# Performance work log

Measured on AMD Instinct MI355X. Metric: run time of the kernel, lower is better.

The kernel has to match this reference:

```python
import jax, jax.numpy as jnp
import numpy as np

NUM_HEADS = 16
HEAD_DIM = 64
WINDOW = 128        # local attention radius |i-j| <= WINDOW
GLOBAL_STRIDE = 64  # tokens at multiples of GLOBAL_STRIDE attend/are attended globally
NEG_INF = -1e9


def sparse_mask(seq_len):
    # bool [S, S]: local band plus global rows/cols (Longformer-style pattern)
    i = jnp.arange(seq_len)
    local = jnp.abs(i[:, None] - i[None, :]) <= WINDOW
    is_global = (i % GLOBAL_STRIDE) == 0
    return local | is_global[:, None] | is_global[None, :]


def setup_inputs() -> dict:
    key = jax.random.key(0)
    k1, k2, k3 = jax.random.split(key, 3)
    B, S, H = 1, 2048, 1024
    x = jax.random.normal(k1, (B, S, H), dtype=jnp.float32)
    Wqkv = jax.random.normal(k2, (3 * H, H), dtype=jnp.float32) * (1.0 / np.sqrt(H))
    Wout = jax.random.normal(k3, (H, H), dtype=jnp.float32) * (1.0 / np.sqrt(H))
    return {"x": x, "Wqkv": Wqkv, "Wout": Wout}


def reference(x, Wqkv, Wout):
    B, S, H = x.shape
    hd = HEAD_DIM
    scale = 1.0 / np.sqrt(hd)

    qkv = x @ Wqkv.T                       # [B, S, 3H] (torch Linear: x @ W^T)
    q, k, v = jnp.split(qkv, 3, axis=-1)
    # [B, nH, S, hd]
    q = q.reshape(B, S, NUM_HEADS, hd).transpose(0, 2, 1, 3)
    k = k.reshape(B, S, NUM_HEADS, hd).transpose(0, 2, 1, 3)
    v = v.reshape(B, S, NUM_HEADS, hd).transpose(0, 2, 1, 3)

    mask = sparse_mask(S)                  # [S, S] bool, broadcasts over (B, nH)
    scores = jnp.einsum('bhqd,bhkd->bhqk', q, k) * scale
    scores = jnp.where(mask, scores, NEG_INF)
    attn = jax.nn.softmax(scores, axis=-1)  # every row has valid keys -> no NaN
    out = jnp.einsum('bhqk,bhkd->bhqd', attn, v)
    out = out.transpose(0, 2, 1, 3).reshape(B, S, H)
    return out @ Wout.T
```

## Files before the change

kernel.cpp:

```cpp
#include <hip/hip_runtime.h>
#include <hip/hip_bf16.h>
#include <math.h>

#define SEQ   2048
#define HID   1024
#define NH    16
#define HD    64
#define WIN   128
#define GSTR  64

typedef __attribute__((ext_vector_type(8))) short short8;
typedef __attribute__((ext_vector_type(4))) float f32x4;
typedef unsigned short ushort_t;

__device__ inline unsigned short bf16b(float f) {
    union { float f; unsigned int u; } v; v.f = f;
    return (unsigned short)((v.u + 0x7FFFu + ((v.u >> 16) & 1u)) >> 16);
}
__device__ inline float blo(unsigned int u) {
    union { unsigned int i; float f; } v; v.i = u << 16; return v.f;
}
__device__ inline float bhi(unsigned int u) {
    union { unsigned int i; float f; } v; v.i = u & 0xFFFF0000u; return v.f;
}

#define GLOAD_LDS16(gp, lp)                                                    \
    __builtin_amdgcn_global_load_lds(                                          \
        (const __attribute__((address_space(1))) unsigned int*)(gp),           \
        (__attribute__((address_space(3))) unsigned int*)(lp), 16, 0, 0)

__global__ __launch_bounds__(256) void cvt_bf16(const float4* __restrict__ x,
                                                const float4* __restrict__ wq,
                                                const float4* __restrict__ wo,
                                                ushort4* __restrict__ x16,
                                                ushort4* __restrict__ wq16,
                                                ushort4* __restrict__ wo16) {
    for (int idx = blockIdx.x * 256 + threadIdx.x; idx < 1572864;
         idx += gridDim.x * 256) {
        const float4* src; ushort4* dst; int off;
        if (idx < 524288)       { src = x;  dst = x16;  off = idx; }
        else if (idx < 1310720) { src = wq; dst = wq16; off = idx - 524288; }
        else                    { src = wo; dst = wo16; off = idx - 1310720; }
        float4 v = src[off];
        ushort4 o;
        o.x = bf16b(v.x); o.y = bf16b(v.y); o.z = bf16b(v.z); o.w = bf16b(v.w);
        dst[off] = o;
    }
}

template <int BM, int BN, typename OT>
__global__ __launch_bounds__(256) void gemm_bt16(const unsigned short* __restrict__ A,
                                                 const unsigned short* __restrict__ B,
                                                 OT* __restrict__ C,
                                                 int M, int N, int K) {
    constexpr int MI = BM / 32;
    constexpr int NJ = BN / 32;
    __shared__ unsigned short As[2][BM * 32];
    __shared__ unsigned short Bs[2][BN * 32];

    const int tid  = threadIdx.x;
    const int wave = tid >> 6;
    const int lane = tid & 63;
    const int quad = lane >> 4;
    const int l15  = lane & 15;
    const int bm = blockIdx.y * BM;
    const int bn = blockIdx.x * BN;
    const int wm = (wave & 1) * (BM / 2);
    const int wn = (wave >> 1) * (BN / 2);
    const int srow = lane >> 2;
    const int scol = (lane & 3) * 8;

    f32x4 acc[MI][NJ];
    #pragma unroll
    for (int i = 0; i < MI; ++i)
        #pragma unroll
        for (int j = 0; j < NJ; ++j)
            acc[i][j] = (f32x4){0.f, 0.f, 0.f, 0.f};

    for (int k0 = 0; k0 < K; k0 += 64) {
        #pragma unroll
        for (int hh = 0; hh < 2; ++hh) {
            #pragma unroll
            for (int t = 0; t < BM / 64; ++t) {
                const int row = wave * (BM / 4) + t * 16 + srow;
                GLOAD_LDS16(A + (size_t)(bm + row) * K + k0 + hh * 32 + scol,
                            &As[hh][(size_t)row * 32 + scol]);
            }
            #pragma unroll
            for (int t = 0; t < BN / 64; ++t) {
                const int row = wave * (BN / 4) + t * 16 + srow;
                GLOAD_LDS16(B + (size_t)(bn + row) * K + k0 + hh * 32 + scol,
                            &Bs[hh][(size_t)row * 32 + scol]);
            }
        }
        __syncthreads();

        #pragma unroll
        for (int hh = 0; hh < 2; ++hh) {
            short8 a[MI], b[NJ];
            #pragma unroll
            for (int im = 0; im < MI; ++im)
                a[im] = *(const short8*)&As[hh][(wm + im * 16 + l15) * 32 + quad * 8];
            #pragma unroll
            for (int jn = 0; jn < NJ; ++jn)
                b[jn] = *(const short8*)&Bs[hh][(wn + jn * 16 + l15) * 32 + quad * 8];

            #pragma unroll
            for (int im = 0; im < MI; ++im)
                #pragma unroll
                for (int jn = 0; jn < NJ; ++jn)
                    acc[im][jn] = __builtin_amdgcn_mfma_f32_16x16x32_bf16(
                        b[jn], a[im], acc[im][jn], 0, 0, 0);
        }
        __syncthreads();
    }

    #pragma unroll
    for (int im = 0; im < MI; ++im)
        #pragma unroll
        for (int jn = 0; jn < NJ; ++jn) {
            const int r = bm + wm + im * 16 + l15;
            const int c = bn + wn + jn * 16 + quad * 4;
            if constexpr (sizeof(OT) == 2) {
                ushort4 o;
                o.x = bf16b(acc[im][jn][0]);
                o.y = bf16b(acc[im][jn][1]);
                o.z = bf16b(acc[im][jn][2]);
                o.w = bf16b(acc[im][jn][3]);
                *(ushort4*)&C[(size_t)r * N + c] = o;
            } else {
                *(f32x4*)&C[(size_t)r * N + c] = acc[im][jn];
            }
        }
}

__global__ __launch_bounds__(256) void attn_fused(const unsigned short* __restrict__ qkv16,
                                                  unsigned short* __restrict__ aout16) {
    __shared__ __align__(16) unsigned char smem[38912];
    const int tid = threadIdx.x;
    const int h = blockIdx.y;
    const int w    = tid >> 6;
    const int lane = tid & 63;
    const int quad = lane >> 4;
    const int l15  = lane & 15;

    if (blockIdx.x < 32) {
        ushort_t* Qs = (ushort_t*)smem;
        ushort_t* Ks = (ushort_t*)(smem + 9216);
        ushort_t* Vt = (ushort_t*)(smem + 18432);
        ushort_t* Ps = (ushort_t*)(smem + 27648);

        const int bq = blockIdx.x;
        const int q0 = bq * 64;
        const int qi = q0 + w * 16 + l15;

        for (int f = tid; f < 512; f += 256) {
            int row = f >> 3, c8 = f & 7;
            *(uint4*)&Qs[row * 72 + c8 * 8] =
                *(const uint4*)&qkv16[(size_t)(q0 + row) * (3 * HID) + h * HD + c8 * 8];
        }

        float mq = -1.0e30f, lq = 0.f;
        f32x4 Oacc[4];
        #pragma unroll
        for (int jt = 0; jt < 4; ++jt) Oacc[jt] = (f32x4){0.f, 0.f, 0.f, 0.f};

        const int t0 = max(bq - 2, 0);
        const int t1 = min(bq + 2, SEQ / 64 - 1);

        uint4 pk[2];
        uint2 pva[2], pvb[2];

        auto prefetch = [&](int tt2, bool g2) {
            const int nf = g2 ? 256 : 512;
            #pragma unroll
            for (int u = 0; u < 2; ++u) {
                const int f = tid + u * 256;
                if (f < nf) {
                    const int row = f >> 3, c8 = f & 7;
                    const size_t gb = (size_t)(g2 ? (row << 6) : (tt2 * 64 + row))
                                          * (3 * HID) + HID + h * HD + c8 * 8;
                    pk[u] = *(const uint4*)&qkv16[gb];
                    const int kp = f >> 4, dc = f & 15;
                    const int k0i = 2 * kp, k1i = 2 * kp + 1;
                    const size_t b0 = (size_t)(g2 ? (k0i << 6) : (tt2 * 64 + k0i))
                                          * (3 * HID) + 2 * HID + h * HD + dc * 4;
                    const size_t b1 = (size_t)(g2 ? (k1i << 6) : (tt2 * 64 + k1i))
                                          * (3 * HID) + 2 * HID + h * HD + dc * 4;
                    pva[u] = *(const uint2*)&qkv16[b0];
                    pvb[u] = *(const uint2*)&qkv16[b1];
                }
            }
        };
        auto commit = [&](bool g2) {
            const int nf = g2 ? 256 : 512;
            #pragma unroll
            for (int u = 0; u < 2; ++u) {
                const int f = tid + u * 256;
                if (f < nf) {
                    const int row = f >> 3, c8 = f & 7;
                    *(uint4*)&Ks[row * 72 + c8 * 8] = pk[u];
                    const int kp = f >> 4, dc = f & 15;
                    uint2 va = pva[u], vb = pvb[u];
                    unsigned int w0 = (va.x & 0xFFFFu) | (vb.x << 16);
                    unsigned int w1 = (va.x >> 16)     | (vb.x & 0xFFFF0000u);
                    unsigned int w2 = (va.y & 0xFFFFu) | (vb.y << 16);
                    unsigned int w3 = (va.y >> 16)     | (vb.y & 0xFFFF0000u);
                    *(unsigned int*)&Vt[(dc * 4 + 0) * 72 + 2 * kp] = w0;
                    *(unsigned int*)&Vt[(dc * 4 + 1) * 72 + 2 * kp] = w1;
                    *(unsigned int*)&Vt[(dc * 4 + 2) * 72 + 2 * kp] = w2;
                    *(unsigned int*)&Vt[(dc * 4 + 3) * 72 + 2 * kp] = w3;
                }
            }
        };

        prefetch(t0, false);
        commit(false);
        __syncthreads();

        for (int tt = t0; tt <= t1 + 1; ++tt) {
            const bool gather = (tt == t1 + 1);
            const bool hasnext = (tt < t1 + 1);
            if (hasnext) prefetch(tt + 1, (tt + 1) == t1 + 1);

            short8 bQ0 = *(const short8*)&Qs[(w * 16 + l15) * 72 + quad * 8];
            short8 bQ1 = *(const short8*)&Qs[(w * 16 + l15) * 72 + 32 + quad * 8];
            f32x4 st[4];
            #pragma unroll
            for (int kt = 0; kt < 4; ++kt) {
                short8 aK0 = *(const short8*)&Ks[(kt * 16 + l15) * 72 + quad * 8];
                short8 aK1 = *(const short8*)&Ks[(kt * 16 + l15) * 72 + 32 + quad * 8];
                f32x4 z = (f32x4){0.f, 0.f, 0.f, 0.f};
                z = __builtin_amdgcn_mfma_f32_16x16x32_bf16(aK0, bQ0, z, 0, 0, 0);
                z = __builtin_amdgcn_mfma_f32_16x16x32_bf16(aK1, bQ1, z, 0, 0, 0);
                st[kt] = z;
            }

            float sv[4][4];
            float tm = -1.0e30f;
            #pragma unroll
            for (int kt = 0; kt < 4; ++kt)
                #pragma unroll
                for (int reg = 0; reg < 4; ++reg) {
                    const int c = kt * 16 + quad * 4 + reg;
                    const int j = gather ? (c << 6) : (tt * 64 + c);
                    const bool valid = gather ? ((c < 32) && (abs(qi - j) > WIN))
                                              : (abs(qi - j) <= WIN);
                    sv[kt][reg] = valid ? st[kt][reg] * 0.125f : -1.0e30f;
                    tm = fmaxf(tm, sv[kt][reg]);
                }

            tm = fmaxf(tm, __shfl_xor(tm, 16));
            tm = fmaxf(tm, __shfl_xor(tm, 32));
            const float mn = fmaxf(mq, tm);
            const float alpha = __expf(mq - mn);
            float p[4][4];
            float ts = 0.f;
            #pragma unroll
            for (int kt = 0; kt < 4; ++kt)
                #pragma unroll
                for (int reg = 0; reg < 4; ++reg) {
                    p[kt][reg] = __expf(sv[kt][reg] - mn);
                    ts += p[kt][reg];
                }
            ts += __shfl_xor(ts, 16);
            ts += __shfl_xor(ts, 32);
            lq = lq * alpha + ts;
            mq = mn;

            #pragma unroll
            for (int kt = 0; kt < 4; ++kt) {
                ushort4 pkt;
                pkt.x = bf16b(p[kt][0]); pkt.y = bf16b(p[kt][1]);
                pkt.z = bf16b(p[kt][2]); pkt.w = bf16b(p[kt][3]);
                *(ushort4*)&Ps[(w * 16 + l15) * 72 + kt * 16 + quad * 4] = pkt;
            }
            #pragma unroll
            for (int jt = 0; jt < 4; ++jt) {
                Oacc[jt][0] *= alpha; Oacc[jt][1] *= alpha;
                Oacc[jt][2] *= alpha; Oacc[jt][3] *= alpha;
            }

            short8 bP0 = *(const short8*)&Ps[(w * 16 + l15) * 72 + quad * 8];
            short8 bP1 = *(const short8*)&Ps[(w * 16 + l15) * 72 + 32 + quad * 8];
            #pragma unroll
            for (int jt = 0; jt < 4; ++jt) {
                short8 aV0 = *(const short8*)&Vt[(jt * 16 + l15) * 72 + quad * 8];
                short8 aV1 = *(const short8*)&Vt[(jt * 16 + l15) * 72 + 32 + quad * 8];
                Oacc[jt] = __builtin_amdgcn_mfma_f32_16x16x32_bf16(aV0, bP0, Oacc[jt], 0, 0, 0);
                Oacc[jt] = __builtin_amdgcn_mfma_f32_16x16x32_bf16(aV1, bP1, Oacc[jt], 0, 0, 0);
            }

            if (hasnext) {
                __syncthreads();
                commit((tt + 1) == t1 + 1);
                __syncthreads();
            }
        }

        if (!(w == 0 && l15 == 0)) {
            const float inv = 1.0f / lq;
            #pragma unroll
            for (int jt = 0; jt < 4; ++jt) {
                ushort4 o;
                o.x = bf16b(Oacc[jt][0] * inv);
                o.y = bf16b(Oacc[jt][1] * inv);
                o.z = bf16b(Oacc[jt][2] * inv);
                o.w = bf16b(Oacc[jt][3] * inv);
                *(ushort4*)&aout16[(size_t)qi * HID + h * HD + jt * 16 + quad * 4] = o;
            }
        }
    } else {
        const int gh = blockIdx.x - 32;
        ushort_t* Ksw = (ushort_t*)(smem + w * 9728);
        ushort_t* Vtw = (ushort_t*)(smem + w * 9728 + 4608);
        ushort_t* Psw = (ushort_t*)(smem + w * 9728 + 8704);

        const size_t qrow = (size_t)((gh * 16 + l15) * 64) * (3 * HID) + h * HD;
        short8 bQ0 = *(const short8*)&qkv16[qrow + quad * 8];
        short8 bQ1 = *(const short8*)&qkv16[qrow + 32 + quad * 8];

        float mq = -1.0e30f, lq = 0.f;
        f32x4 Oacc[4];
        #pragma unroll
        for (int jt = 0; jt < 4; ++jt) Oacc[jt] = (f32x4){0.f, 0.f, 0.f, 0.f};

        for (int s = 0; s < 16; ++s) {
            const int kb = w * 512 + s * 32;
            #pragma unroll
            for (int u = 0; u < 4; ++u) {
                const int unit = lane + u * 64;
                const int row = unit >> 3, c8 = unit & 7;
                *(uint4*)&Ksw[row * 72 + c8 * 8] =
                    *(const uint4*)&qkv16[(size_t)(kb + row) * (3 * HID) + HID + h * HD + c8 * 8];
            }
            #pragma unroll
            for (int u = 0; u < 4; ++u) {
                const int unit = lane + u * 64;
                const int kp = unit >> 4, dc = unit & 15;
                const size_t b0 = (size_t)(kb + 2 * kp) * (3 * HID) + 2 * HID + h * HD + dc * 4;
                const size_t b1 = b0 + 3 * HID;
                uint2 va = *(const uint2*)&qkv16[b0];
                uint2 vb = *(const uint2*)&qkv16[b1];
                unsigned int w0 = (va.x & 0xFFFFu) | (vb.x << 16);
                unsigned int w1 = (va.x >> 16)     | (vb.x & 0xFFFF0000u);
                unsigned int w2 = (va.y & 0xFFFFu) | (vb.y << 16);
                unsigned int w3 = (va.y >> 16)     | (vb.y & 0xFFFF0000u);
                *(unsigned int*)&Vtw[(dc * 4 + 0) * 32 + 2 * kp] = w0;
                *(unsigned int*)&Vtw[(dc * 4 + 1) * 32 + 2 * kp] = w1;
                *(unsigned int*)&Vtw[(dc * 4 + 2) * 32 + 2 * kp] = w2;
                *(unsigned int*)&Vtw[(dc * 4 + 3) * 32 + 2 * kp] = w3;
            }

            f32x4 st[2];
            #pragma unroll
            for (int kt = 0; kt < 2; ++kt) {
                short8 aK0 = *(const short8*)&Ksw[(kt * 16 + l15) * 72 + quad * 8];
                short8 aK1 = *(const short8*)&Ksw[(kt * 16 + l15) * 72 + 32 + quad * 8];
                f32x4 z = (f32x4){0.f, 0.f, 0.f, 0.f};
                z = __builtin_amdgcn_mfma_f32_16x16x32_bf16(aK0, bQ0, z, 0, 0, 0);
                z = __builtin_amdgcn_mfma_f32_16x16x32_bf16(aK1, bQ1, z, 0, 0, 0);
                st[kt] = z;
            }

            float sv[2][4];
            float tm = -1.0e30f;
            #pragma unroll
            for (int kt = 0; kt < 2; ++kt)
                #pragma unroll
                for (int reg = 0; reg < 4; ++reg) {
                    sv[kt][reg] = st[kt][reg] * 0.125f;
                    tm = fmaxf(tm, sv[kt][reg]);
                }
            tm = fmaxf(tm, __shfl_xor(tm, 16));
            tm = fmaxf(tm, __shfl_xor(tm, 32));
            const float mn = fmaxf(mq, tm);
            const float alpha = __expf(mq - mn);
            float p[2][4];
            float ts = 0.f;
            #pragma unroll
            for (int kt = 0; kt < 2; ++kt)
                #pragma unroll
                for (int reg = 0; reg < 4; ++reg) {
                    p[kt][reg] = __expf(sv[kt][reg] - mn);
                    ts += p[kt][reg];
                }
            ts += __shfl_xor(ts, 16);
            ts += __shfl_xor(ts, 32);
            lq = lq * alpha + ts;
            mq = mn;

            #pragma unroll
            for (int kt = 0; kt < 2; ++kt) {
                ushort4 pkt;
                pkt.x = bf16b(p[kt][0]); pkt.y = bf16b(p[kt][1]);
                pkt.z = bf16b(p[kt][2]); pkt.w = bf16b(p[kt][3]);
                *(ushort4*)&Psw[l15 * 32 + kt * 16 + quad * 4] = pkt;
            }
            #pragma unroll
            for (int jt = 0; jt < 4; ++jt) {
                Oacc[jt][0] *= alpha; Oacc[jt][1] *= alpha;
                Oacc[jt][2] *= alpha; Oacc[jt][3] *= alpha;
            }

            short8 bP = *(const short8*)&Psw[l15 * 32 + quad * 8];
            #pragma unroll
            for (int jt = 0; jt < 4; ++jt) {
                short8 aV = *(const short8*)&Vtw[(jt * 16 + l15) * 32 + quad * 8];
                Oacc[jt] = __builtin_amdgcn_mfma_f32_16x16x32_bf16(aV, bP, Oacc[jt], 0, 0, 0);
            }
        }

        __syncthreads();
        float* Om = (float*)smem;
        float* Ml = (float*)(smem + 16384);
        float* Ll = (float*)(smem + 16640);
        #pragma unroll
        for (int jt = 0; jt < 4; ++jt)
            #pragma unroll
            for (int reg = 0; reg < 4; ++reg)
                Om[(w * 16 + l15) * 64 + jt * 16 + quad * 4 + reg] = Oacc[jt][reg];
        if (quad == 0) { Ml[w * 16 + l15] = mq; Ll[w * 16 + l15] = lq; }
        __syncthreads();

        const int d = tid & 63;
        #pragma unroll
        for (int k = 0; k < 4; ++k) {
            const int q = (tid >> 6) * 4 + k;
            float m0 = Ml[q], m1 = Ml[16 + q], m2 = Ml[32 + q], m3 = Ml[48 + q];
            float mM = fmaxf(fmaxf(m0, m1), fmaxf(m2, m3));
            float e0 = __expf(m0 - mM), e1 = __expf(m1 - mM);
            float e2 = __expf(m2 - mM), e3 = __expf(m3 - mM);
            float l = e0 * Ll[q] + e1 * Ll[16 + q] + e2 * Ll[32 + q] + e3 * Ll[48 + q];
            float o = e0 * Om[(q) * 64 + d]        + e1 * Om[(16 + q) * 64 + d]
                    + e2 * Om[(32 + q) * 64 + d]   + e3 * Om[(48 + q) * 64 + d];
            const int i = (gh * 16 + q) * 64;
            aout16[(size_t)i * HID + h * HD + d] = bf16b(o / l);
        }
    }
}

extern "C" void kernel_launch(void* const* d_in, const int* in_sizes, int n_in,
                              void* d_out, int out_size, void* d_ws, size_t ws_size,
                              hipStream_t stream) {
    const float* x    = (const float*)d_in[0];
    const float* Wqkv = (const float*)d_in[1];
    const float* Wout = (const float*)d_in[2];
    float* out = (float*)d_out;

    unsigned short* x16    = (unsigned short*)d_ws;
    unsigned short* wq16   = x16  + (size_t)SEQ * HID;
    unsigned short* wo16   = wq16 + (size_t)3 * HID * HID;
    unsigned short* qkv16  = wo16 + (size_t)HID * HID;
    unsigned short* aout16 = qkv16 + (size_t)SEQ * 3 * HID;

    cvt_bf16<<<dim3(1024), 256, 0, stream>>>(
        (const float4*)x, (const float4*)Wqkv, (const float4*)Wout,
        (ushort4*)x16, (ushort4*)wq16, (ushort4*)wo16);

    gemm_bt16<128, 128, unsigned short><<<dim3(3 * HID / 128, SEQ / 128), 256, 0, stream>>>(
        x16, wq16, qkv16, SEQ, 3 * HID, HID);

    attn_fused<<<dim3(34, NH), 256, 0, stream>>>(qkv16, aout16);

    gemm_bt16<64, 64, float><<<dim3(HID / 64, SEQ / 64), 256, 0, stream>>>(
        aout16, wo16, out, SEQ, HID, HID);
}
```

Before: 150.3 us.

## Split global-row attention across key chunks with separate combine kernel

Measured after the change: 141.6 us. -5.8%, faster.

```diff
diff --git a/kernel.cpp b/kernel.cpp
--- a/kernel.cpp
+++ b/kernel.cpp
@@ -8,6 +8,7 @@
 #define HD    64
 #define WIN   128
 #define GSTR  64
+#define NSPL  8
 
 typedef __attribute__((ext_vector_type(8))) short short8;
 typedef __attribute__((ext_vector_type(4))) float f32x4;
@@ -16,12 +17,6 @@
 __device__ inline unsigned short bf16b(float f) {
     union { float f; unsigned int u; } v; v.f = f;
     return (unsigned short)((v.u + 0x7FFFu + ((v.u >> 16) & 1u)) >> 16);
-}
-__device__ inline float blo(unsigned int u) {
-    union { unsigned int i; float f; } v; v.i = u << 16; return v.f;
-}
-__device__ inline float bhi(unsigned int u) {
-    union { unsigned int i; float f; } v; v.i = u & 0xFFFF0000u; return v.f;
 }
 
 #define GLOAD_LDS16(gp, lp)                                                    \
@@ -135,7 +130,10 @@
 }
 
 __global__ __launch_bounds__(256) void attn_fused(const unsigned short* __restrict__ qkv16,
-                                                  unsigned short* __restrict__ aout16) {
+                                                  unsigned short* __restrict__ aout16,
+                                                  float* __restrict__ pO,
+                                                  float* __restrict__ pM,
+                                                  float* __restrict__ pL) {
     __shared__ __align__(16) unsigned char smem[38912];
     const int tid = threadIdx.x;
     const int h = blockIdx.y;
@@ -311,7 +309,9 @@
             }
         }
     } else {
-        const int gh = blockIdx.x - 32;
+        const int sid = blockIdx.x - 32;
+        const int gh  = sid / NSPL;
+        const int sp  = sid % NSPL;
         ushort_t* Ksw = (ushort_t*)(smem + w * 9728);
         ushort_t* Vtw = (ushort_t*)(smem + w * 9728 + 4608);
         ushort_t* Psw = (ushort_t*)(smem + w * 9728 + 8704);
@@ -325,8 +325,9 @@
         #pragma unroll
         for (int jt = 0; jt < 4; ++jt) Oacc[jt] = (f32x4){0.f, 0.f, 0.f, 0.f};
 
-        for (int s = 0; s < 16; ++s) {
-            const int kb = w * 512 + s * 32;
+        #pragma unroll
+        for (int s = 0; s < 2; ++s) {
+            const int kb = sp * 256 + w * 64 + s * 32;
             #pragma unroll
             for (int u = 0; u < 4; ++u) {
                 const int unit = lane + u * 64;
@@ -339,9 +340,8 @@
                 const int unit = lane + u * 64;
                 const int kp = unit >> 4, dc = unit & 15;
                 const size_t b0 = (size_t)(kb + 2 * kp) * (3 * HID) + 2 * HID + h * HD + dc * 4;
-                const size_t b1 = b0 + 3 * HID;
                 uint2 va = *(const uint2*)&qkv16[b0];
-                uint2 vb = *(const uint2*)&qkv16[b1];
+                uint2 vb = *(const uint2*)&qkv16[b0 + 3 * HID];
                 unsigned int w0 = (va.x & 0xFFFFu) | (vb.x << 16);
                 unsigned int w1 = (va.x >> 16)     | (vb.x & 0xFFFF0000u);
                 unsigned int w2 = (va.y & 0xFFFFu) | (vb.y << 16);
@@ -423,6 +423,7 @@
         if (quad == 0) { Ml[w * 16 + l15] = mq; Ll[w * 16 + l15] = lq; }
         __syncthreads();
 
+        const int pt = (h * 2 + gh) * NSPL + sp;
         const int d = tid & 63;
         #pragma unroll
         for (int k = 0; k < 4; ++k) {
@@ -434,9 +435,36 @@
             float l = e0 * Ll[q] + e1 * Ll[16 + q] + e2 * Ll[32 + q] + e3 * Ll[48 + q];
             float o = e0 * Om[(q) * 64 + d]        + e1 * Om[(16 + q) * 64 + d]
                     + e2 * Om[(32 + q) * 64 + d]   + e3 * Om[(48 + q) * 64 + d];
-            const int i = (gh * 16 + q) * 64;
-            aout16[(size_t)i * HID + h * HD + d] = bf16b(o / l);
-        }
+            pO[(size_t)pt * 1024 + q * 64 + d] = o;
+            if (d == 0) { pM[pt * 16 + q] = mM; pL[pt * 16 + q] = l; }
+        }
+    }
+}
+
+__global__ __launch_bounds__(256) void attn_combine(const float* __restrict__ pO,
+                                                    const float* __restrict__ pM,
+                                                    const float* __restrict__ pL,
+                                                    unsigned short* __restrict__ aout16) {
+    const int bid = blockIdx.x;
+    const int h = bid >> 1, gh = bid & 1;
+    const int base = (h * 2 + gh) * NSPL;
+    #pragma unroll
+    for (int k = 0; k < 4; ++k) {
+        const int idx = threadIdx.x + k * 256;
+        const int q = idx >> 6, d = idx & 63;
+        float mM = -1.0e30f;
+        #pragma unroll
+        for (int sp = 0; sp < NSPL; ++sp)
+            mM = fmaxf(mM, pM[(base + sp) * 16 + q]);
+        float l = 0.f, o = 0.f;
+        #pragma unroll
+        for (int sp = 0; sp < NSPL; ++sp) {
+            const float e = __expf(pM[(base + sp) * 16 + q] - mM);
+            l += e * pL[(base + sp) * 16 + q];
+            o += e * pO[(size_t)(base + sp) * 1024 + q * 64 + d];
+        }
+        const int row = (gh * 16 + q) * 64;
+        aout16[(size_t)row * HID + h * HD + d] = bf16b(o / l);
     }
 }
 
@@ -453,15 +481,20 @@
     unsigned short* wo16   = wq16 + (size_t)3 * HID * HID;
     unsigned short* qkv16  = wo16 + (size_t)HID * HID;
     unsigned short* aout16 = qkv16 + (size_t)SEQ * 3 * HID;
+    float* pO = (float*)(aout16 + (size_t)SEQ * HID);
+    float* pM = pO + (size_t)NH * 2 * NSPL * 1024;
+    float* pL = pM + (size_t)NH * 2 * NSPL * 16;
 
     cvt_bf16<<<dim3(1024), 256, 0, stream>>>(
         (const float4*)x, (const float4*)Wqkv, (const float4*)Wout,
         (ushort4*)x16, (ushort4*)wq16, (ushort4*)wo16);
 
-    gemm_bt16<128, 128, unsigned short><<<dim3(3 * HID / 128, SEQ / 128), 256, 0, stream>>>(
+    gemm_bt16<64, 128, unsigned short><<<dim3(3 * HID / 128, SEQ / 64), 256, 0, stream>>>(
         x16, wq16, qkv16, SEQ, 3 * HID, HID);
 
-    attn_fused<<<dim3(34, NH), 256, 0, stream>>>(qkv16, aout16);
+    attn_fused<<<dim3(32 + 2 * NSPL, NH), 256, 0, stream>>>(
+        qkv16, aout16, pO, pM, pL);
+    attn_combine<<<dim3(32), 256, 0, stream>>>(pO, pM, pL, aout16);
 
     gemm_bt16<64, 64, float><<<dim3(HID / 64, SEQ / 64), 256, 0, stream>>>(
         aout16, wo16, out, SEQ, HID, HID);
```
